# Optimization experiments

Measured on AMD Instinct MI355X. Metric: run time of the kernel, lower is better.

## Reference

```python
import jax, jax.numpy as jnp
import numpy as np

D_MODEL = 1024
H = 16
D_K = D_MODEL // H
NEG = -1e9


def setup_inputs() -> dict:
    key = jax.random.key(0)
    ks = jax.random.split(key, 12)
    B, S = 2, 2048
    sc = 1.0 / np.sqrt(D_MODEL)
    inp = {
        'query': jax.random.normal(ks[0], (B, S, D_MODEL), jnp.float32),
        'key': jax.random.normal(ks[1], (B, S, D_MODEL), jnp.float32),
        'value': jax.random.normal(ks[2], (B, S, D_MODEL), jnp.float32),
        'Wq': jax.random.normal(ks[3], (D_MODEL, D_MODEL), jnp.float32) * sc,
        'bq': jnp.zeros((D_MODEL,), jnp.float32),
        'Wk': jax.random.normal(ks[4], (D_MODEL, D_MODEL), jnp.float32) * sc,
        'bk': jnp.zeros((D_MODEL,), jnp.float32),
        'Wv': jax.random.normal(ks[5], (D_MODEL, D_MODEL), jnp.float32) * sc,
        'bv': jnp.zeros((D_MODEL,), jnp.float32),
        'Wo': jax.random.normal(ks[6], (D_MODEL, D_MODEL), jnp.float32) * sc,
        'bo': jnp.zeros((D_MODEL,), jnp.float32),
        'raw_thresholds': jnp.full((H, 1, 1), 0.1, jnp.float32),
    }
    return inp


def _softplus_t(x):
    # nn.Softplus(beta=1, threshold=20)
    return jnp.where(x > 20.0, x, jax.nn.softplus(x))


def reference(query, key, value, Wq, bq, Wk, bk, Wv, bv, Wo, bo, raw_thresholds):
    B, S, _ = query.shape
    # projections + split heads: [B, H, S, D_K]
    def proj(x, W, b):
        return (x @ W.T + b).reshape(B, -1, H, D_K).transpose(0, 2, 1, 3)
    Q = proj(query, Wq, bq)
    K = proj(key, Wk, bk)
    V = proj(value, Wv, bv)
    scores = jnp.einsum('bhqd,bhkd->bhqk', Q, K) / jnp.sqrt(jnp.float32(D_K))
    thr = _softplus_t(raw_thresholds)[None]  # [1, H, 1, 1]
    scores = jnp.where(scores <= thr, NEG, scores)
    attn = jax.nn.softmax(scores, axis=-1)
    x = jnp.einsum('bhqk,bhkd->bhqd', attn, V)
    x = x.transpose(0, 2, 1, 3).reshape(B, S, H * D_K)
    return x @ Wo.T + bo
```

## Files before the change

### kernel.cpp

```cpp
#include <hip/hip_runtime.h>
#include <hip/hip_bf16.h>

typedef _Float16 f16;
typedef __attribute__((ext_vector_type(8))) f16 h8;
typedef __attribute__((ext_vector_type(4))) float f32x4;
typedef __attribute__((ext_vector_type(8))) short short8;

static __device__ __forceinline__ short h2s(f16 h) { return __builtin_bit_cast(short, h); }

#define BM 128
#define BK 32
#define PREMUL 0.18033688011112042f

__global__ __launch_bounds__(256) void cvt_kernel(
    const float* __restrict__ q, const float* __restrict__ k, const float* __restrict__ v,
    const float* __restrict__ Wq, const float* __restrict__ Wk, const float* __restrict__ Wv,
    const float* __restrict__ Wo,
    short* __restrict__ Xqh, short* __restrict__ Xkh, short* __restrict__ Xvh,
    short* __restrict__ Wqh, short* __restrict__ Wkh,
    short* __restrict__ Wvh, short* __restrict__ Woh) {
    const int z = blockIdx.y;
    const int n = (z < 3) ? (1 << 22) : (1 << 20);
    const int idx = (blockIdx.x * 256 + threadIdx.x) * 8;
    if (idx >= n) return;
    const float* src = z == 0 ? q : z == 1 ? k : z == 2 ? v : z == 3 ? Wq : z == 4 ? Wk : z == 5 ? Wv : Wo;
    short* dh = z == 0 ? Xqh : z == 1 ? Xkh : z == 2 ? Xvh : z == 3 ? Wqh : z == 4 ? Wkh : z == 5 ? Wvh : Woh;
    const float4 a = *(const float4*)(src + idx);
    const float4 b = *(const float4*)(src + idx + 4);
    float f[8] = {a.x, a.y, a.z, a.w, b.x, b.y, b.z, b.w};
    short8 hi;
#pragma unroll
    for (int j = 0; j < 8; ++j) hi[j] = h2s((f16)f[j]);
    *(short8*)(dh + idx) = hi;
}

template <int EPI>
static __device__ __forceinline__ void gemm16(const short* __restrict__ Ag,
                                              const short* __restrict__ Bhg,
                                              const float* __restrict__ bias,
                                              short* __restrict__ o0,
                                              float* __restrict__ of) {
    extern __shared__ __align__(16) short smem[];
    constexpr int SETSZ = 2 * BM * BK;

    const int K = 1024;
    const int tid = threadIdx.x;
    const int lane = tid & 63;
    const int w = tid >> 6;
    const int lr = lane & 15, lg = lane >> 4;
    const int wm = (w & 1) * 64, wn = (w >> 1) * 64;
    const int m0 = blockIdx.x * BM, n0 = blockIdx.y * BM;

    const int lane2 = lane >> 2;
    const int slot8 = (lane & 3) * 8;

    f32x4 acc[4][4] = {};

    const int NT = K / BK;

    auto STAGE = [&](int set, int t) {
        const int ko = t * BK;
        short* Ah = smem + set * SETSZ;
        short* Bh = Ah + BM * BK;
#pragma unroll
        for (int i = 0; i < 2; ++i) {
            const int r = i * 64 + w * 16 + lane2;
            const int ldsoff = i * 4096 + w * 1024;
            __builtin_amdgcn_global_load_lds(Ag + (size_t)(m0 + r) * K + ko + slot8,
                                             (char*)Ah + ldsoff, 16, 0, 0);
            __builtin_amdgcn_global_load_lds(Bhg + (size_t)(n0 + r) * K + ko + slot8,
                                             (char*)Bh + ldsoff, 16, 0, 0);
        }
    };

    auto COMPUTE = [&](int set) {
        const short* Ah = smem + set * SETSZ;
        const short* Bh = Ah + BM * BK;
        h8 afh[4], bfh[4];
#pragma unroll
        for (int f = 0; f < 4; ++f) {
            afh[f] = *(const h8*)&Ah[(wm + f * 16 + lr) * BK + lg * 8];
            bfh[f] = *(const h8*)&Bh[(wn + f * 16 + lr) * BK + lg * 8];
        }
        __builtin_amdgcn_s_setprio(1);
#pragma unroll
        for (int i = 0; i < 4; i++)
#pragma unroll
            for (int j = 0; j < 4; j++)
                acc[i][j] = __builtin_amdgcn_mfma_f32_16x16x32_f16(afh[i], bfh[j], acc[i][j], 0, 0, 0);
        __builtin_amdgcn_s_setprio(0);
    };

    STAGE(0, 0);
    STAGE(1, 1);
    asm volatile("s_waitcnt vmcnt(4) lgkmcnt(0)" ::: "memory");
    __builtin_amdgcn_s_barrier();
    int cur = 0, nxt2 = 2;
    for (int t = 0; t < NT; ++t) {
        if (t + 2 < NT) STAGE(nxt2, t + 2);
        COMPUTE(cur);
        if (t + 2 < NT)
            asm volatile("s_waitcnt vmcnt(4) lgkmcnt(0)" ::: "memory");
        else
            asm volatile("s_waitcnt vmcnt(0) lgkmcnt(0)" ::: "memory");
        __builtin_amdgcn_s_barrier();
        cur = (cur == 2) ? 0 : cur + 1;
        nxt2 = (nxt2 == 2) ? 0 : nxt2 + 1;
    }

#pragma unroll
    for (int fn = 0; fn < 4; ++fn) {
        const int n = n0 + wn + fn * 16 + lr;
        const float bia = bias[n];
#pragma unroll
        for (int fm = 0; fm < 4; ++fm) {
#pragma unroll
            for (int i = 0; i < 4; i++) {
                const int m = m0 + wm + fm * 16 + lg * 4 + i;
                float val = acc[fm][fn][i] + bia;
                if (EPI == 0) {
                    of[(size_t)m * 1024 + n] = val;
                } else {
                    const int bb = m >> 11, s = m & 2047, hh = n >> 6, d = n & 63;
                    if (EPI == 2 || EPI == 4) {
                        if (EPI == 4) val *= PREMUL;
                        const size_t off = (((size_t)(bb * 16 + hh) * 2048 + s) << 6) + d;
                        o0[off] = h2s((f16)val);
                    } else {
                        const size_t off = ((size_t)(bb * 16 + hh) * 64 + d) * 2048 + s;
                        o0[off] = h2s((f16)val);
                    }
                }
            }
        }
    }
}

__global__ __launch_bounds__(256) void qkv_kernel(
    const short* __restrict__ Xqh, const short* __restrict__ Xkh, const short* __restrict__ Xvh,
    const short* __restrict__ Wqh, const short* __restrict__ Wkh, const short* __restrict__ Wvh,
    const float* __restrict__ bq, const float* __restrict__ bk, const float* __restrict__ bv,
    short* __restrict__ Qh, short* __restrict__ Kh, short* __restrict__ Vt_g) {
    if (blockIdx.z == 0)
        gemm16<4>(Xqh, Wqh, bq, Qh, nullptr);
    else if (blockIdx.z == 1)
        gemm16<2>(Xkh, Wkh, bk, Kh, nullptr);
    else
        gemm16<3>(Xvh, Wvh, bv, Vt_g, nullptr);
}

__global__ __launch_bounds__(256) void oproj_kernel(const short* __restrict__ Xb,
                                                    const short* __restrict__ Woh,
                                                    const float* __restrict__ bo,
                                                    float* __restrict__ out) {
    gemm16<0>(Xb, Woh, bo, nullptr, out);
}

#define PSK 76
__global__ __launch_bounds__(512) void attn_kernel(const short* __restrict__ Qh,
                                                   const short* __restrict__ Kh,
                                                   const short* __restrict__ Vg,
                                                   const float* __restrict__ rawthr,
                                                   short* __restrict__ Xb) {
    __shared__ __align__(16) short Ksh[2][64][72];
    __shared__ __align__(16) short Vt[2][64][72];
    __shared__ __align__(16) short Ps[8][16][PSK];
    const int tid = threadIdx.x, lane = tid & 63, w = tid >> 6;
    const int lr = lane & 15, lg = lane >> 4;
    const int bh = blockIdx.y;
    const int b = bh >> 4, h = bh & 15;
    const size_t base = (size_t)bh * 2048 * 64;
    const float LOG2E = 1.4426950408889634f;
    const float rt = rawthr[h];
    const float thr = rt > 20.f ? rt : log1pf(expf(rt));
    const float thr2 = thr * LOG2E;
    const int qrow = blockIdx.x * 128 + w * 16;

    h8 qf[2];
#pragma unroll
    for (int kk = 0; kk < 2; ++kk)
        qf[kk] = *(const h8*)(Qh + base + (size_t)(qrow + lr) * 64 + kk * 32 + lg * 8);

    f32x4 acc[4] = {};
    float lpart = 0.f;

    const int skey = tid >> 3;
    const int sfe = (tid & 7) * 8;
    short8 khreg, vreg;
    {
        khreg = *(const short8*)(Kh + base + (size_t)skey * 64 + sfe);
        vreg = *(const short8*)(Vg + base + (size_t)skey * 2048 + sfe);
        *(short8*)&Ksh[0][skey][sfe] = khreg;
        *(short8*)&Vt[0][skey][sfe] = vreg;
    }
    __syncthreads();

    for (int kt = 0; kt < 32; ++kt) {
        const int cur = kt & 1;
        const bool more = (kt + 1 < 32);
        if (more) {
            khreg = *(const short8*)(Kh + base + (size_t)((kt + 1) * 64 + skey) * 64 + sfe);
            vreg = *(const short8*)(Vg + base + (size_t)skey * 2048 + (kt + 1) * 64 + sfe);
        }
        f32x4 sc[4] = {};
        __builtin_amdgcn_s_setprio(1);
#pragma unroll
        for (int fn = 0; fn < 4; ++fn) {
#pragma unroll
            for (int kk = 0; kk < 2; ++kk) {
                const h8 khf = *(const h8*)&Ksh[cur][fn * 16 + lr][kk * 32 + lg * 8];
                sc[fn] = __builtin_amdgcn_mfma_f32_16x16x32_f16(khf, qf[kk], sc[fn], 0, 0, 0);
            }
        }
        __builtin_amdgcn_s_setprio(0);
#pragma unroll
        for (int fn = 0; fn < 4; ++fn)
#pragma unroll
            for (int i = 0; i < 4; ++i) {
                float s = sc[fn][i];
                s = (s <= thr2) ? -1e30f : s;
                const float p = __builtin_amdgcn_exp2f(s);
                sc[fn][i] = p;
                lpart += p;
            }
#pragma unroll
        for (int fn = 0; fn < 4; ++fn) {
            const unsigned int p01 =
                __builtin_bit_cast(unsigned int, __builtin_amdgcn_cvt_pkrtz(sc[fn][0], sc[fn][1]));
            const unsigned int p23 =
                __builtin_bit_cast(unsigned int, __builtin_amdgcn_cvt_pkrtz(sc[fn][2], sc[fn][3]));
            uint2 u;
            u.x = p01;
            u.y = p23;
            *(uint2*)&Ps[w][lr][fn * 16 + lg * 4] = u;
        }
        h8 pa[2];
#pragma unroll
        for (int kk = 0; kk < 2; ++kk)
            pa[kk] = *(const h8*)&Ps[w][lr][kk * 32 + lg * 8];
        __builtin_amdgcn_s_setprio(1);
#pragma unroll
        for (int kk = 0; kk < 2; ++kk)
#pragma unroll
            for (int fv = 0; fv < 4; ++fv) {
                const h8 vf = *(const h8*)&Vt[cur][fv * 16 + lr][kk * 32 + lg * 8];
                acc[fv] = __builtin_amdgcn_mfma_f32_16x16x32_f16(pa[kk], vf, acc[fv], 0, 0, 0);
            }
        __builtin_amdgcn_s_setprio(0);
        if (more) {
            *(short8*)&Ksh[cur ^ 1][skey][sfe] = khreg;
            *(short8*)&Vt[cur ^ 1][skey][sfe] = vreg;
        }
        __syncthreads();
    }
    float lrun = lpart;
    lrun += __shfl_xor(lrun, 16);
    lrun += __shfl_xor(lrun, 32);
#pragma unroll
    for (int i = 0; i < 4; ++i) {
        const float lq = __shfl(lrun, lg * 4 + i);
        const float inv = 1.f / lq;
        const int s = qrow + lg * 4 + i;
#pragma unroll
        for (int fv = 0; fv < 4; ++fv) {
            const int d = fv * 16 + lr;
            Xb[((size_t)(b * 2048 + s) << 10) + (h << 6) + d] = h2s((f16)(acc[fv][i] * inv));
        }
    }
}

extern "C" void kernel_launch(void* const* d_in, const int* in_sizes, int n_in,
                              void* d_out, int out_size, void* d_ws, size_t ws_size,
                              hipStream_t stream) {
    const float* q = (const float*)d_in[0];
    const float* k = (const float*)d_in[1];
    const float* v = (const float*)d_in[2];
    const float* Wq = (const float*)d_in[3];
    const float* bq = (const float*)d_in[4];
    const float* Wk = (const float*)d_in[5];
    const float* bk = (const float*)d_in[6];
    const float* Wv = (const float*)d_in[7];
    const float* bv = (const float*)d_in[8];
    const float* Wo = (const float*)d_in[9];
    const float* bo = (const float*)d_in[10];
    const float* thr = (const float*)d_in[11];
    float* out = (float*)d_out;

    const size_t MX = (size_t)4 * 1024 * 1024;
    const size_t MW = (size_t)1024 * 1024;
    short* Xqh = (short*)d_ws;
    short* Xkh = Xqh + MX;
    short* Xvh = Xkh + MX;
    short* Wqh = Xvh + MX;
    short* Wkh = Wqh + MW;
    short* Wvh = Wkh + MW;
    short* Woh = Wvh + MW;
    short* Qh = Woh + MW;
    short* Kh = Qh + MX;
    short* Vt = Kh + MX;
    short* Xb = Xkh;

    const size_t LDS_GEMM = 3 * 2 * BM * BK * sizeof(short);

    cvt_kernel<<<dim3(2048, 7), 256, 0, stream>>>(q, k, v, Wq, Wk, Wv, Wo,
                                                  Xqh, Xkh, Xvh,
                                                  Wqh, Wkh, Wvh, Woh);
    qkv_kernel<<<dim3(32, 8, 3), 256, LDS_GEMM, stream>>>(Xqh, Xkh, Xvh,
                                                          Wqh, Wkh, Wvh,
                                                          bq, bk, bv, Qh, Kh, Vt);
    attn_kernel<<<dim3(16, 32), 512, 0, stream>>>(Qh, Kh, Vt, thr, Xb);
    oproj_kernel<<<dim3(32, 8), 256, LDS_GEMM, stream>>>(Xb, Woh, bo, out);
}
```

Baseline: 125.3 us.

## Split attention over key range into two halves with a merge kernel

Attention blocks now each process half the key tiles (grid z=2) and write unnormalized fp32 partial outputs and row sums. A new merge kernel adds the two partials, normalizes, and writes the fp16 head-interleaved buffer. This doubles block count to improve CU utilization, at the cost of extra global traffic for fp32 partials and an added launch. The K/V LDS staging is also changed from double to single buffering with two barriers per tile.

```diff
diff --git a/kernel.cpp b/kernel.cpp
--- a/kernel.cpp
+++ b/kernel.cpp
@@ -161,20 +161,25 @@
                                                    const short* __restrict__ Kh,
                                                    const short* __restrict__ Vg,
                                                    const float* __restrict__ rawthr,
-                                                   short* __restrict__ Xb) {
-    __shared__ __align__(16) short Ksh[2][64][72];
-    __shared__ __align__(16) short Vt[2][64][72];
+                                                   float* __restrict__ P0, float* __restrict__ P1,
+                                                   float* __restrict__ L0, float* __restrict__ L1) {
+    __shared__ __align__(16) short Ksh[64][72];
+    __shared__ __align__(16) short Vt[64][72];
     __shared__ __align__(16) short Ps[8][16][PSK];
     const int tid = threadIdx.x, lane = tid & 63, w = tid >> 6;
     const int lr = lane & 15, lg = lane >> 4;
     const int bh = blockIdx.y;
-    const int b = bh >> 4, h = bh & 15;
+    const int z = blockIdx.z;
+    const int t0 = z * 16;
+    const int h = bh & 15;
     const size_t base = (size_t)bh * 2048 * 64;
     const float LOG2E = 1.4426950408889634f;
     const float rt = rawthr[h];
     const float thr = rt > 20.f ? rt : log1pf(expf(rt));
     const float thr2 = thr * LOG2E;
     const int qrow = blockIdx.x * 128 + w * 16;
+    float* __restrict__ Pz = z ? P1 : P0;
+    float* __restrict__ Lz = z ? L1 : L0;
 
     h8 qf[2];
 #pragma unroll
@@ -188,17 +193,16 @@
     const int sfe = (tid & 7) * 8;
     short8 khreg, vreg;
     {
-        khreg = *(const short8*)(Kh + base + (size_t)skey * 64 + sfe);
-        vreg = *(const short8*)(Vg + base + (size_t)skey * 2048 + sfe);
-        *(short8*)&Ksh[0][skey][sfe] = khreg;
-        *(short8*)&Vt[0][skey][sfe] = vreg;
-    }
-    __syncthreads();
-
-    for (int kt = 0; kt < 32; ++kt) {
-        const int cur = kt & 1;
-        const bool more = (kt + 1 < 32);
-        if (more) {
+        khreg = *(const short8*)(Kh + base + (size_t)(t0 * 64 + skey) * 64 + sfe);
+        vreg = *(const short8*)(Vg + base + (size_t)skey * 2048 + t0 * 64 + sfe);
+    }
+
+    for (int kt = t0; kt < t0 + 16; ++kt) {
+        __syncthreads();
+        *(short8*)&Ksh[skey][sfe] = khreg;
+        *(short8*)&Vt[skey][sfe] = vreg;
+        __syncthreads();
+        if (kt + 1 < t0 + 16) {
             khreg = *(const short8*)(Kh + base + (size_t)((kt + 1) * 64 + skey) * 64 + sfe);
             vreg = *(const short8*)(Vg + base + (size_t)skey * 2048 + (kt + 1) * 64 + sfe);
         }
@@ -208,7 +212,7 @@
         for (int fn = 0; fn < 4; ++fn) {
 #pragma unroll
             for (int kk = 0; kk < 2; ++kk) {
-                const h8 khf = *(const h8*)&Ksh[cur][fn * 16 + lr][kk * 32 + lg * 8];
+                const h8 khf = *(const h8*)&Ksh[fn * 16 + lr][kk * 32 + lg * 8];
                 sc[fn] = __builtin_amdgcn_mfma_f32_16x16x32_f16(khf, qf[kk], sc[fn], 0, 0, 0);
             }
         }
@@ -243,30 +247,47 @@
         for (int kk = 0; kk < 2; ++kk)
 #pragma unroll
             for (int fv = 0; fv < 4; ++fv) {
-                const h8 vf = *(const h8*)&Vt[cur][fv * 16 + lr][kk * 32 + lg * 8];
+                const h8 vf = *(const h8*)&Vt[fv * 16 + lr][kk * 32 + lg * 8];
                 acc[fv] = __builtin_amdgcn_mfma_f32_16x16x32_f16(pa[kk], vf, acc[fv], 0, 0, 0);
             }
         __builtin_amdgcn_s_setprio(0);
-        if (more) {
-            *(short8*)&Ksh[cur ^ 1][skey][sfe] = khreg;
-            *(short8*)&Vt[cur ^ 1][skey][sfe] = vreg;
-        }
-        __syncthreads();
     }
     float lrun = lpart;
     lrun += __shfl_xor(lrun, 16);
     lrun += __shfl_xor(lrun, 32);
+    if (lg == 0) Lz[bh * 2048 + qrow + lr] = lrun;
 #pragma unroll
     for (int i = 0; i < 4; ++i) {
-        const float lq = __shfl(lrun, lg * 4 + i);
-        const float inv = 1.f / lq;
         const int s = qrow + lg * 4 + i;
 #pragma unroll
         for (int fv = 0; fv < 4; ++fv) {
             const int d = fv * 16 + lr;
-            Xb[((size_t)(b * 2048 + s) << 10) + (h << 6) + d] = h2s((f16)(acc[fv][i] * inv));
-        }
-    }
+            Pz[(((size_t)(bh * 2048 + s)) << 6) + d] = acc[fv][i];
+        }
+    }
+}
+
+__global__ __launch_bounds__(256) void merge_kernel(const float* __restrict__ P0,
+                                                    const float* __restrict__ P1,
+                                                    const float* __restrict__ L0,
+                                                    const float* __restrict__ L1,
+                                                    short* __restrict__ Xb) {
+    const int t = blockIdx.x * 256 + threadIdx.x;
+    const int row = t >> 3;
+    const int c8 = (t & 7) * 8;
+    const float inv = 1.f / (L0[row] + L1[row]);
+    const size_t po = (size_t)row * 64 + c8;
+    const float4 a0 = *(const float4*)(P0 + po);
+    const float4 a1 = *(const float4*)(P0 + po + 4);
+    const float4 b0 = *(const float4*)(P1 + po);
+    const float4 b1 = *(const float4*)(P1 + po + 4);
+    float vsum[8] = {a0.x + b0.x, a0.y + b0.y, a0.z + b0.z, a0.w + b0.w,
+                     a1.x + b1.x, a1.y + b1.y, a1.z + b1.z, a1.w + b1.w};
+    short8 o;
+#pragma unroll
+    for (int j = 0; j < 8; ++j) o[j] = h2s((f16)(vsum[j] * inv));
+    const int bb = row >> 15, hh = (row >> 11) & 15, s = row & 2047;
+    *(short8*)(Xb + (((size_t)(bb * 2048 + s)) << 10) + (hh << 6) + c8) = o;
 }
 
 extern "C" void kernel_launch(void* const* d_in, const int* in_sizes, int n_in,
@@ -288,17 +309,21 @@
 
     const size_t MX = (size_t)4 * 1024 * 1024;
     const size_t MW = (size_t)1024 * 1024;
-    short* Xqh = (short*)d_ws;
+    short* Woh = (short*)d_ws;
+    short* Xqh = Woh + MW;
     short* Xkh = Xqh + MX;
     short* Xvh = Xkh + MX;
     short* Wqh = Xvh + MX;
     short* Wkh = Wqh + MW;
     short* Wvh = Wkh + MW;
-    short* Woh = Wvh + MW;
-    short* Qh = Woh + MW;
+    short* Qh = Wvh + MW;
     short* Kh = Qh + MX;
     short* Vt = Kh + MX;
-    short* Xb = Xkh;
+    float* P1 = (float*)(Vt + MX);
+    short* Xb = (short*)(P1 + MX);
+    float* L0 = (float*)(Xb + MX);
+    float* L1 = L0 + 65536;
+    float* P0 = (float*)Xqh;
 
     const size_t LDS_GEMM = 3 * 2 * BM * BK * sizeof(short);
 
@@ -308,6 +333,7 @@
     qkv_kernel<<<dim3(32, 8, 3), 256, LDS_GEMM, stream>>>(Xqh, Xkh, Xvh,
                                                           Wqh, Wkh, Wvh,
                                                           bq, bk, bv, Qh, Kh, Vt);
-    attn_kernel<<<dim3(16, 32), 512, 0, stream>>>(Qh, Kh, Vt, thr, Xb);
+    attn_kernel<<<dim3(16, 32, 2), 512, 0, stream>>>(Qh, Kh, Vt, thr, P0, P1, L0, L1);
+    merge_kernel<<<dim3(2048), 256, 0, stream>>>(P0, P1, L0, L1, Xb);
     oproj_kernel<<<dim3(32, 8), 256, LDS_GEMM, stream>>>(Xb, Woh, bo, out);
 }
```

Result: slower. 135.0 us (+7.7%).
